# Optimization experiments

Measured on AMD Instinct MI355X. Metric: run time of the kernel, lower is better.

Reference implementation:

```python
import jax, jax.numpy as jnp
import numpy as np

N = 100000   # nodes
E = 800000   # edges
P = 100000   # pos/neg pairs
H = 4        # heads
IN = 128     # input feature dim
HID = 32     # per-head out dim (H*HID = 128)


def gat_layer(h, src, dst, W, al, ar, b):
    """DGL-style GATConv: gather -> leaky_relu attention -> segment softmax -> scatter."""
    n = h.shape[0]
    nh, nf = al.shape
    feat = (h @ W).reshape(n, nh, nf)                       # [N,H,F]
    el = jnp.einsum('nhf,hf->nh', feat, al)                 # [N,H]
    er = jnp.einsum('nhf,hf->nh', feat, ar)                 # [N,H]
    e = jax.nn.leaky_relu(el[src] + er[dst], negative_slope=0.2)  # [E,H]
    emax = jax.ops.segment_max(e, dst, num_segments=n)      # [N,H]
    emax = jnp.where(jnp.isfinite(emax), emax, 0.0)         # zero-in-degree guard
    w = jnp.exp(e - emax[dst])                              # [E,H]
    denom = jax.ops.segment_sum(w, dst, num_segments=n)     # [N,H]
    alpha = w / jnp.maximum(denom[dst], 1e-9)               # [E,H]
    out = jax.ops.segment_sum(feat[src] * alpha[:, :, None], dst, num_segments=n)  # [N,H,F]
    return out.reshape(n, nh * nf) + b


def setup_inputs() -> dict:
    key = jax.random.key(0)
    ks = jax.random.split(key, 32)
    s = 0.1
    d = {
        'x': jax.random.normal(ks[0], (N, IN), jnp.float32),
        'src': jax.random.randint(ks[1], (E,), 0, N),
        'dst': jax.random.randint(ks[2], (E,), 0, N),
        'pos_src': jax.random.randint(ks[3], (P,), 0, N),
        'pos_dst': jax.random.randint(ks[4], (P,), 0, N),
        'neg_src': jax.random.randint(ks[5], (P,), 0, N),
        'neg_dst': jax.random.randint(ks[6], (P,), 0, N),
    }
    HF = H * HID
    # 3 GATConv layers, all 128 -> 4x32
    for l in range(3):
        ind = IN if l == 0 else HF
        d[f'W{l}'] = s * jax.random.normal(ks[7 + 4 * l], (ind, HF), jnp.float32)
        d[f'al{l}'] = s * jax.random.normal(ks[8 + 4 * l], (H, HID), jnp.float32)
        d[f'ar{l}'] = s * jax.random.normal(ks[9 + 4 * l], (H, HID), jnp.float32)
        d[f'b{l}'] = jnp.zeros((HF,), jnp.float32)
    # projection 128 -> 32
    d['Wp'] = s * jax.random.normal(ks[20], (HF, HID), jnp.float32)
    d['bp'] = jnp.zeros((HID,), jnp.float32)
    # predictor MLP 32 -> 32 -> 32 -> 1
    d['Wq1'] = s * jax.random.normal(ks[21], (HID, HID), jnp.float32)
    d['bq1'] = jnp.zeros((HID,), jnp.float32)
    d['Wq2'] = s * jax.random.normal(ks[22], (HID, HID), jnp.float32)
    d['bq2'] = jnp.zeros((HID,), jnp.float32)
    d['Wq3'] = s * jax.random.normal(ks[23], (HID, 1), jnp.float32)
    d['bq3'] = jnp.zeros((1,), jnp.float32)
    return d


def reference(x, src, dst, pos_src, pos_dst, neg_src, neg_dst,
              W0, al0, ar0, b0, W1, al1, ar1, b1, W2, al2, ar2, b2,
              Wp, bp, Wq1, bq1, Wq2, bq2, Wq3, bq3):
    h = x
    for W, al, ar, b in ((W0, al0, ar0, b0), (W1, al1, ar1, b1), (W2, al2, ar2, b2)):
        h = jax.nn.elu(gat_layer(h, src, dst, W, al, ar, b))
    h = h @ Wp + bp                                          # [N,HID]

    def predictor(z):
        z = jax.nn.relu(z @ Wq1 + bq1)
        z = jax.nn.relu(z @ Wq2 + bq2)
        return z @ Wq3 + bq3

    h_pos = predictor(h[pos_src] * h[pos_dst])               # [P,1]
    h_neg = predictor(h[neg_src] * h[neg_dst])               # [P,1]
    return (h_pos, h_neg)
```

## Files before the change

kernel.cpp:

```cpp
#include <hip/hip_runtime.h>
#include <math.h>

__global__ __launch_bounds__(256) void hist_k(const int* __restrict__ dst, int* __restrict__ deg, int e) {
    int i = blockIdx.x * 256 + threadIdx.x;
    if (i < e) atomicAdd(&deg[dst[i]], 1);
}

__global__ __launch_bounds__(256) void scan1_k(const int* __restrict__ deg, int* __restrict__ rowptr,
                                               int* __restrict__ bsum, int n) {
    __shared__ int sh[256];
    int tid = threadIdx.x;
    int sid = blockIdx.x * 256 + tid;
    int v = (sid < n) ? deg[sid] : 0;
    sh[tid] = v; __syncthreads();
    for (int off = 1; off < 256; off <<= 1) {
        int t = (tid >= off) ? sh[tid - off] : 0;
        __syncthreads();
        sh[tid] += t;
        __syncthreads();
    }
    if (sid < n) rowptr[sid + 1] = sh[tid];
    if (tid == 255) bsum[blockIdx.x] = sh[255];
}

__global__ __launch_bounds__(512) void scan2_k(int* __restrict__ bsum, int nb) {
    __shared__ int sh[512];
    int tid = threadIdx.x;
    sh[tid] = (tid < nb) ? bsum[tid] : 0;
    __syncthreads();
    for (int off = 1; off < 512; off <<= 1) {
        int t = (tid >= off) ? sh[tid - off] : 0;
        __syncthreads();
        sh[tid] += t;
        __syncthreads();
    }
    if (tid < nb) bsum[tid] = sh[tid];
}

__global__ __launch_bounds__(256) void scan3_k(int* __restrict__ rowptr, const int* __restrict__ bsum, int n) {
    int sid = blockIdx.x * 256 + threadIdx.x;
    if (sid == 0) rowptr[0] = 0;
    if (sid < n && blockIdx.x > 0) rowptr[sid + 1] += bsum[blockIdx.x - 1];
}

__global__ __launch_bounds__(256) void fill_k(const int* __restrict__ src, const int* __restrict__ dst,
                                              const int* __restrict__ rowptr, int* __restrict__ cursor,
                                              int* __restrict__ csrc, int* __restrict__ cdst, int e) {
    int i = blockIdx.x * 256 + threadIdx.x;
    if (i < e) {
        int d = dst[i];
        int pos = rowptr[d] + atomicAdd(&cursor[d], 1);
        csrc[pos] = src[i];
        cdst[pos] = d;
    }
}

__global__ __launch_bounds__(256) void gemm_feat_k(const float* __restrict__ A, const float* __restrict__ W,
                                                   const float* __restrict__ al, const float* __restrict__ ar,
                                                   float* __restrict__ C, float* __restrict__ el,
                                                   float* __restrict__ er, int M) {
    __shared__ float As[32][132];
    __shared__ float Bs[32][128];
    int tid = threadIdx.x;
    int m0 = blockIdx.x * 128;
    int tr = tid >> 4;
    int tc = tid & 15;
    float4 alA = *(const float4*)(al + tc * 4);
    float4 alB = *(const float4*)(al + 64 + tc * 4);
    float4 arA = *(const float4*)(ar + tc * 4);
    float4 arB = *(const float4*)(ar + 64 + tc * 4);
    float acc[8][8];
    #pragma unroll
    for (int i = 0; i < 8; i++)
        #pragma unroll
        for (int j = 0; j < 8; j++) acc[i][j] = 0.f;

    int arow = tid >> 3, acg = tid & 7;
    int bkr = tid >> 5, bcg = tid & 31;

    for (int kb = 0; kb < 128; kb += 32) {
        #pragma unroll
        for (int rp = 0; rp < 4; ++rp) {
            int m = m0 + arow + rp * 32;
            int mm = min(m, M - 1);
            float4 a4 = *(const float4*)(A + (size_t)mm * 128 + kb + acg * 4);
            As[acg * 4 + 0][arow + rp * 32] = a4.x;
            As[acg * 4 + 1][arow + rp * 32] = a4.y;
            As[acg * 4 + 2][arow + rp * 32] = a4.z;
            As[acg * 4 + 3][arow + rp * 32] = a4.w;
        }
        #pragma unroll
        for (int rp = 0; rp < 4; ++rp) {
            int k = kb + bkr + rp * 8;
            *(float4*)&Bs[bkr + rp * 8][bcg * 4] = *(const float4*)(W + (size_t)k * 128 + bcg * 4);
        }
        __syncthreads();
        #pragma unroll
        for (int k = 0; k < 32; ++k) {
            float a[8], b[8];
            *(float4*)(a)     = *(float4*)&As[k][tr * 4];
            *(float4*)(a + 4) = *(float4*)&As[k][64 + tr * 4];
            *(float4*)(b)     = *(float4*)&Bs[k][tc * 4];
            *(float4*)(b + 4) = *(float4*)&Bs[k][64 + tc * 4];
            #pragma unroll
            for (int i = 0; i < 8; i++)
                #pragma unroll
                for (int j = 0; j < 8; j++) acc[i][j] += a[i] * b[j];
        }
        __syncthreads();
    }
    #pragma unroll
    for (int i = 0; i < 8; i++) {
        int m = m0 + ((i < 4) ? (tr * 4 + i) : (64 + tr * 4 + (i - 4)));
        if (m < M) {
            *(float4*)(C + (size_t)m * 128 + tc * 4)      = make_float4(acc[i][0], acc[i][1], acc[i][2], acc[i][3]);
            *(float4*)(C + (size_t)m * 128 + 64 + tc * 4) = make_float4(acc[i][4], acc[i][5], acc[i][6], acc[i][7]);
        }
    }
    #pragma unroll
    for (int i = 0; i < 8; i++) {
        float plA = acc[i][0] * alA.x + acc[i][1] * alA.y + acc[i][2] * alA.z + acc[i][3] * alA.w;
        float plB = acc[i][4] * alB.x + acc[i][5] * alB.y + acc[i][6] * alB.z + acc[i][7] * alB.w;
        float prA = acc[i][0] * arA.x + acc[i][1] * arA.y + acc[i][2] * arA.z + acc[i][3] * arA.w;
        float prB = acc[i][4] * arB.x + acc[i][5] * arB.y + acc[i][6] * arB.z + acc[i][7] * arB.w;
        #pragma unroll
        for (int off = 1; off < 8; off <<= 1) {
            plA += __shfl_xor(plA, off);
            plB += __shfl_xor(plB, off);
            prA += __shfl_xor(prA, off);
            prB += __shfl_xor(prB, off);
        }
        if ((tc & 7) == 0) {
            int m = m0 + ((i < 4) ? (tr * 4 + i) : (64 + tr * 4 + (i - 4)));
            if (m < M) {
                int hA = tc >> 3;
                el[m * 4 + hA]     = plA;
                el[m * 4 + hA + 2] = plB;
                er[m * 4 + hA]     = prA;
                er[m * 4 + hA + 2] = prB;
            }
        }
    }
}

__global__ __launch_bounds__(256) void edgew_k(const int* __restrict__ csrc, const int* __restrict__ cdst,
                                               const float* __restrict__ el, const float* __restrict__ er,
                                               float* __restrict__ wbuf, int e) {
    int p = blockIdx.x * 256 + threadIdx.x;
    if (p >= e) return;
    int s = csrc[p], d = cdst[p];
    float4 l4 = *(const float4*)(el + (size_t)s * 4);
    float4 r4 = *(const float4*)(er + (size_t)d * 4);
    float e0 = l4.x + r4.x, e1 = l4.y + r4.y, e2 = l4.z + r4.z, e3 = l4.w + r4.w;
    e0 = (e0 > 0.f) ? e0 : 0.2f * e0;
    e1 = (e1 > 0.f) ? e1 : 0.2f * e1;
    e2 = (e2 > 0.f) ? e2 : 0.2f * e2;
    e3 = (e3 > 0.f) ? e3 : 0.2f * e3;
    *(float4*)(wbuf + (size_t)p * 4) = make_float4(__expf(e0), __expf(e1), __expf(e2), __expf(e3));
}

__global__ __launch_bounds__(256) void aggregate_k(const float* __restrict__ feat, const float* __restrict__ wbuf,
                                                   const int* __restrict__ rowptr, const int* __restrict__ csrc,
                                                   const float* __restrict__ bias, float* __restrict__ out, int n) {
    int wid = threadIdx.x >> 6;
    int lane = threadIdx.x & 63;
    int node = blockIdx.x * 4 + wid;
    if (node >= n) return;
    int h = lane >> 4;
    int p0 = rowptr[node], p1 = rowptr[node + 1];
    float2 b2 = *(const float2*)(bias + lane * 2);
    float lsum = 0.f, a0 = 0.f, a1 = 0.f;
    int p = p0;
    for (; p + 4 <= p1; p += 4) {
        int s0 = csrc[p], s1 = csrc[p + 1], s2 = csrc[p + 2], s3 = csrc[p + 3];
        float w0 = wbuf[(size_t)p * 4 + h];
        float w1 = wbuf[(size_t)(p + 1) * 4 + h];
        float w2 = wbuf[(size_t)(p + 2) * 4 + h];
        float w3 = wbuf[(size_t)(p + 3) * 4 + h];
        float2 f0 = *(const float2*)(feat + (size_t)s0 * 128 + lane * 2);
        float2 f1 = *(const float2*)(feat + (size_t)s1 * 128 + lane * 2);
        float2 f2 = *(const float2*)(feat + (size_t)s2 * 128 + lane * 2);
        float2 f3 = *(const float2*)(feat + (size_t)s3 * 128 + lane * 2);
        lsum += (w0 + w1) + (w2 + w3);
        a0 += w0 * f0.x + w1 * f1.x + w2 * f2.x + w3 * f3.x;
        a1 += w0 * f0.y + w1 * f1.y + w2 * f2.y + w3 * f3.y;
    }
    for (; p < p1; ++p) {
        int s = csrc[p];
        float w = wbuf[(size_t)p * 4 + h];
        float2 f = *(const float2*)(feat + (size_t)s * 128 + lane * 2);
        lsum += w;
        a0 += w * f.x;
        a1 += w * f.y;
    }
    float inv = 1.f / fmaxf(lsum, 1e-9f);
    float v0 = a0 * inv + b2.x;
    float v1 = a1 * inv + b2.y;
    v0 = (v0 > 0.f) ? v0 : expm1f(v0);
    v1 = (v1 > 0.f) ? v1 : expm1f(v1);
    *(float2*)(out + (size_t)node * 128 + lane * 2) = make_float2(v0, v1);
}

__global__ __launch_bounds__(256) void proj_k(const float* __restrict__ h, const float* __restrict__ Wp,
                                              const float* __restrict__ bp, float* __restrict__ hp, int n) {
    __shared__ float Ws[128 * 32];
    __shared__ float Hs[32][132];
    int tid = threadIdx.x;
    for (int i = tid; i < 4096; i += 256) Ws[i] = Wp[i];
    int n0 = blockIdx.x * 32;
    for (int i = tid; i < 1024; i += 256) {
        int r = i >> 5, c4 = i & 31;
        int node = n0 + r;
        float4 v = (node < n) ? *(const float4*)(h + (size_t)node * 128 + c4 * 4)
                              : make_float4(0.f, 0.f, 0.f, 0.f);
        *(float4*)&Hs[r][c4 * 4] = v;
    }
    __syncthreads();
    int r = tid >> 3;
    int node = n0 + r;
    int j0 = (tid & 7) * 4;
    if (node < n) {
        float a0 = bp[j0], a1 = bp[j0 + 1], a2 = bp[j0 + 2], a3 = bp[j0 + 3];
        #pragma unroll
        for (int k = 0; k < 128; k++) {
            float av = Hs[r][k];
            float4 w = *(const float4*)&Ws[k * 32 + j0];
            a0 += av * w.x; a1 += av * w.y; a2 += av * w.z; a3 += av * w.w;
        }
        *(float4*)(hp + (size_t)node * 32 + j0) = make_float4(a0, a1, a2, a3);
    }
}

__global__ __launch_bounds__(256) void predictor_k(const float* __restrict__ hp,
                                                   const int* __restrict__ ps, const int* __restrict__ pd,
                                                   const int* __restrict__ ns, const int* __restrict__ nd,
                                                   const float* __restrict__ Wq1, const float* __restrict__ bq1,
                                                   const float* __restrict__ Wq2, const float* __restrict__ bq2,
                                                   const float* __restrict__ Wq3, const float* __restrict__ bq3,
                                                   float* __restrict__ out, int P) {
    __shared__ float w1[1024], w2[1024], w3[32], b1[32], b2[32];
    int tid = threadIdx.x;
    for (int i = tid; i < 1024; i += 256) { w1[i] = Wq1[i]; w2[i] = Wq2[i]; }
    if (tid < 32) { w3[tid] = Wq3[tid]; b1[tid] = bq1[tid]; b2[tid] = bq2[tid]; }
    __syncthreads();
    int gid = blockIdx.x * 256 + tid;
    if (gid >= 2 * P) return;
    int i = (gid < P) ? gid : gid - P;
    int a = (gid < P) ? ps[i] : ns[i];
    int b = (gid < P) ? pd[i] : nd[i];
    float z[32];
    const float4* ha = (const float4*)(hp + (size_t)a * 32);
    const float4* hb = (const float4*)(hp + (size_t)b * 32);
    #pragma unroll
    for (int q = 0; q < 8; q++) {
        float4 x = ha[q], y = hb[q];
        z[q * 4 + 0] = x.x * y.x; z[q * 4 + 1] = x.y * y.y;
        z[q * 4 + 2] = x.z * y.z; z[q * 4 + 3] = x.w * y.w;
    }
    float z1[32];
    #pragma unroll
    for (int j = 0; j < 32; j++) {
        float s = b1[j];
        #pragma unroll
        for (int k = 0; k < 32; k++) s += z[k] * w1[k * 32 + j];
        z1[j] = fmaxf(s, 0.f);
    }
    #pragma unroll
    for (int j = 0; j < 32; j++) {
        float s = b2[j];
        #pragma unroll
        for (int k = 0; k < 32; k++) s += z1[k] * w2[k * 32 + j];
        z[j] = fmaxf(s, 0.f);
    }
    float s3 = bq3[0];
    #pragma unroll
    for (int j = 0; j < 32; j++) s3 += z[j] * w3[j];
    out[gid] = s3;
}

extern "C" void kernel_launch(void* const* d_in, const int* in_sizes, int n_in,
                              void* d_out, int out_size, void* d_ws, size_t ws_size,
                              hipStream_t stream) {
    const float* x   = (const float*)d_in[0];
    const int* src   = (const int*)d_in[1];
    const int* dst   = (const int*)d_in[2];
    const int* psrc  = (const int*)d_in[3];
    const int* pdst  = (const int*)d_in[4];
    const int* nsrc  = (const int*)d_in[5];
    const int* ndst  = (const int*)d_in[6];
    const float* W[3]  = { (const float*)d_in[7],  (const float*)d_in[11], (const float*)d_in[15] };
    const float* al[3] = { (const float*)d_in[8],  (const float*)d_in[12], (const float*)d_in[16] };
    const float* ar[3] = { (const float*)d_in[9],  (const float*)d_in[13], (const float*)d_in[17] };
    const float* bb[3] = { (const float*)d_in[10], (const float*)d_in[14], (const float*)d_in[18] };
    const float* Wp  = (const float*)d_in[19];
    const float* bp  = (const float*)d_in[20];
    const float* Wq1 = (const float*)d_in[21];
    const float* bq1 = (const float*)d_in[22];
    const float* Wq2 = (const float*)d_in[23];
    const float* bq2 = (const float*)d_in[24];
    const float* Wq3 = (const float*)d_in[25];
    const float* bq3 = (const float*)d_in[26];
    float* out = (float*)d_out;

    const int N = in_sizes[0] / 128;
    const int E = in_sizes[1];
    const int P = in_sizes[3];

    size_t off = 0;
    auto alloc = [&](size_t bytes) {
        void* p = (char*)d_ws + off;
        off += (bytes + 255) & ~(size_t)255;
        return p;
    };
    float* bufF  = (float*)alloc((size_t)N * 128 * 4);
    float* bufH  = (float*)alloc((size_t)N * 128 * 4);
    float* elA   = (float*)alloc((size_t)N * 4 * 4);
    float* erA   = (float*)alloc((size_t)N * 4 * 4);
    float* hp    = (float*)alloc((size_t)N * 32 * 4);
    int* rowptr  = (int*)alloc((size_t)(N + 1) * 4);
    int* csrc    = (int*)alloc((size_t)E * 4);
    int* cdst    = (int*)alloc((size_t)E * 4);
    float* wbuf  = (float*)alloc((size_t)E * 4 * 4);
    int* deg     = (int*)alloc((size_t)N * 4);
    int* cursor  = (int*)alloc((size_t)N * 4);
    int* bsum    = (int*)alloc(1024 * 4);
    (void)ws_size;

    const int NB_E = (E + 255) / 256;
    const int NB_N = (N + 255) / 256;

    hipMemsetAsync(deg, 0, (size_t)N * 4, stream);
    hipMemsetAsync(cursor, 0, (size_t)N * 4, stream);

    hist_k<<<NB_E, 256, 0, stream>>>(dst, deg, E);
    scan1_k<<<NB_N, 256, 0, stream>>>(deg, rowptr, bsum, N);
    scan2_k<<<1, 512, 0, stream>>>(bsum, NB_N);
    scan3_k<<<NB_N, 256, 0, stream>>>(rowptr, bsum, N);
    fill_k<<<NB_E, 256, 0, stream>>>(src, dst, rowptr, cursor, csrc, cdst, E);

    const int GEMM_B = (N + 127) / 128;
    const float* hin = x;
    for (int l = 0; l < 3; l++) {
        gemm_feat_k<<<GEMM_B, 256, 0, stream>>>(hin, W[l], al[l], ar[l], bufF, elA, erA, N);
        edgew_k<<<NB_E, 256, 0, stream>>>(csrc, cdst, elA, erA, wbuf, E);
        aggregate_k<<<(N + 3) / 4, 256, 0, stream>>>(bufF, wbuf, rowptr, csrc, bb[l], bufH, N);
        hin = bufH;
    }
    proj_k<<<(N + 31) / 32, 256, 0, stream>>>(bufH, Wp, bp, hp, N);
    predictor_k<<<(2 * P + 255) / 256, 256, 0, stream>>>(hp, psrc, pdst, nsrc, ndst,
                                                         Wq1, bq1, Wq2, bq2, Wq3, bq3, out, P);
}
```

Measured before the change: 558.1 us.

## Halve GEMM tile rows and add register prefetch of next k-tile

The feature GEMM now uses 64-row tiles with 128-thread blocks instead of 128-row tiles with 256 threads. Global loads for the next k-slice of A and W go into registers while the current slice is computed from shared memory. The aim is to hide global load latency and raise occupancy with more, smaller blocks. The cost is more register pressure and twice as many reloads of W across blocks.

```diff
diff --git a/kernel.cpp b/kernel.cpp
--- a/kernel.cpp
+++ b/kernel.cpp
@@ -55,14 +55,14 @@
     }
 }
 
-__global__ __launch_bounds__(256) void gemm_feat_k(const float* __restrict__ A, const float* __restrict__ W,
-                                                   const float* __restrict__ al, const float* __restrict__ ar,
-                                                   float* __restrict__ C, float* __restrict__ el,
-                                                   float* __restrict__ er, int M) {
-    __shared__ float As[32][132];
+__global__ __launch_bounds__(128, 3) void gemm_feat_k(const float* __restrict__ A, const float* __restrict__ W,
+                                                      const float* __restrict__ al, const float* __restrict__ ar,
+                                                      float* __restrict__ C, float* __restrict__ el,
+                                                      float* __restrict__ er, int M) {
+    __shared__ float As[32][68];
     __shared__ float Bs[32][128];
     int tid = threadIdx.x;
-    int m0 = blockIdx.x * 128;
+    int m0 = blockIdx.x * 64;
     int tr = tid >> 4;
     int tc = tid & 15;
     float4 alA = *(const float4*)(al + tc * 4);
@@ -75,31 +75,43 @@
         #pragma unroll
         for (int j = 0; j < 8; j++) acc[i][j] = 0.f;
 
-    int arow = tid >> 3, acg = tid & 7;
+    int arow = tid >> 1, acg = tid & 1;
     int bkr = tid >> 5, bcg = tid & 31;
 
+    int mm = min(m0 + arow, M - 1);
+    const float* Arow = A + (size_t)mm * 128;
+
+    float4 pa[4], pb[8];
+    #pragma unroll
+    for (int j = 0; j < 4; j++) pa[j] = *(const float4*)(Arow + (acg * 4 + j) * 4);
+    #pragma unroll
+    for (int rp = 0; rp < 8; rp++) pb[rp] = *(const float4*)(W + (size_t)(rp * 4 + bkr) * 128 + bcg * 4);
+
     for (int kb = 0; kb < 128; kb += 32) {
         #pragma unroll
-        for (int rp = 0; rp < 4; ++rp) {
-            int m = m0 + arow + rp * 32;
-            int mm = min(m, M - 1);
-            float4 a4 = *(const float4*)(A + (size_t)mm * 128 + kb + acg * 4);
-            As[acg * 4 + 0][arow + rp * 32] = a4.x;
-            As[acg * 4 + 1][arow + rp * 32] = a4.y;
-            As[acg * 4 + 2][arow + rp * 32] = a4.z;
-            As[acg * 4 + 3][arow + rp * 32] = a4.w;
-        }
-        #pragma unroll
-        for (int rp = 0; rp < 4; ++rp) {
-            int k = kb + bkr + rp * 8;
-            *(float4*)&Bs[bkr + rp * 8][bcg * 4] = *(const float4*)(W + (size_t)k * 128 + bcg * 4);
-        }
-        __syncthreads();
+        for (int j = 0; j < 4; j++) {
+            int kr = acg * 16 + j * 4;
+            As[kr + 0][arow] = pa[j].x;
+            As[kr + 1][arow] = pa[j].y;
+            As[kr + 2][arow] = pa[j].z;
+            As[kr + 3][arow] = pa[j].w;
+        }
+        #pragma unroll
+        for (int rp = 0; rp < 8; rp++)
+            *(float4*)&Bs[rp * 4 + bkr][bcg * 4] = pb[rp];
+        __syncthreads();
+        if (kb < 96) {
+            int kn = kb + 32;
+            #pragma unroll
+            for (int j = 0; j < 4; j++) pa[j] = *(const float4*)(Arow + kn + (acg * 4 + j) * 4);
+            #pragma unroll
+            for (int rp = 0; rp < 8; rp++) pb[rp] = *(const float4*)(W + (size_t)(kn + rp * 4 + bkr) * 128 + bcg * 4);
+        }
         #pragma unroll
         for (int k = 0; k < 32; ++k) {
             float a[8], b[8];
             *(float4*)(a)     = *(float4*)&As[k][tr * 4];
-            *(float4*)(a + 4) = *(float4*)&As[k][64 + tr * 4];
+            *(float4*)(a + 4) = *(float4*)&As[k][32 + tr * 4];
             *(float4*)(b)     = *(float4*)&Bs[k][tc * 4];
             *(float4*)(b + 4) = *(float4*)&Bs[k][64 + tc * 4];
             #pragma unroll
@@ -111,7 +123,7 @@
     }
     #pragma unroll
     for (int i = 0; i < 8; i++) {
-        int m = m0 + ((i < 4) ? (tr * 4 + i) : (64 + tr * 4 + (i - 4)));
+        int m = m0 + ((i < 4) ? (tr * 4 + i) : (32 + tr * 4 + (i - 4)));
         if (m < M) {
             *(float4*)(C + (size_t)m * 128 + tc * 4)      = make_float4(acc[i][0], acc[i][1], acc[i][2], acc[i][3]);
             *(float4*)(C + (size_t)m * 128 + 64 + tc * 4) = make_float4(acc[i][4], acc[i][5], acc[i][6], acc[i][7]);
@@ -131,7 +143,7 @@
             prB += __shfl_xor(prB, off);
         }
         if ((tc & 7) == 0) {
-            int m = m0 + ((i < 4) ? (tr * 4 + i) : (64 + tr * 4 + (i - 4)));
+            int m = m0 + ((i < 4) ? (tr * 4 + i) : (32 + tr * 4 + (i - 4)));
             if (m < M) {
                 int hA = tc >> 3;
                 el[m * 4 + hA]     = plA;
@@ -338,10 +350,10 @@
     scan3_k<<<NB_N, 256, 0, stream>>>(rowptr, bsum, N);
     fill_k<<<NB_E, 256, 0, stream>>>(src, dst, rowptr, cursor, csrc, cdst, E);
 
-    const int GEMM_B = (N + 127) / 128;
+    const int GEMM_B = (N + 63) / 64;
     const float* hin = x;
     for (int l = 0; l < 3; l++) {
-        gemm_feat_k<<<GEMM_B, 256, 0, stream>>>(hin, W[l], al[l], ar[l], bufF, elA, erA, N);
+        gemm_feat_k<<<GEMM_B, 128, 0, stream>>>(hin, W[l], al[l], ar[l], bufF, elA, erA, N);
         edgew_k<<<NB_E, 256, 0, stream>>>(csrc, cdst, elA, erA, wbuf, E);
         aggregate_k<<<(N + 3) / 4, 256, 0, stream>>>(bufF, wbuf, rowptr, csrc, bb[l], bufH, N);
         hin = bufH;
```

Result: slower. 1.064 ms (+90.7%).

## Replace FP32 SIMT feature GEMM with split-bf16 MFMA GEMM

Applied to the files above, without the earlier changes.

Replaces the shared-memory FP32 FMA GEMM for the per-layer feature transform with a matrix-core kernel using bf16 MFMA instructions. Accuracy is preserved by splitting both A and W into high and low bf16 parts and issuing three MFMAs per tile (hi*hi, lo*hi, hi*lo). A small kernel pre-converts and transposes W into the two bf16 halves each layer. The attention projections el/er are fused in the epilogue using cross-lane shuffles. This trades extra MFMA work and per-element conversion for moving the GEMM off scalar FMAs, and it drops LDS staging in favour of direct global loads.

```diff
diff --git a/kernel.cpp b/kernel.cpp
--- a/kernel.cpp
+++ b/kernel.cpp
@@ -1,5 +1,14 @@
 #include <hip/hip_runtime.h>
 #include <math.h>
+
+typedef __attribute__((ext_vector_type(8))) short bf16x8;
+typedef __attribute__((ext_vector_type(4))) float f32x4;
+
+__device__ __forceinline__ unsigned short f2bf_rtne(float v) {
+    unsigned u = __float_as_uint(v);
+    u += 0x7FFFu + ((u >> 16) & 1u);
+    return (unsigned short)(u >> 16);
+}
 
 __global__ __launch_bounds__(256) void hist_k(const int* __restrict__ dst, int* __restrict__ deg, int e) {
     int i = blockIdx.x * 256 + threadIdx.x;
@@ -55,89 +64,109 @@
     }
 }
 
-__global__ __launch_bounds__(256) void gemm_feat_k(const float* __restrict__ A, const float* __restrict__ W,
-                                                   const float* __restrict__ al, const float* __restrict__ ar,
-                                                   float* __restrict__ C, float* __restrict__ el,
-                                                   float* __restrict__ er, int M) {
-    __shared__ float As[32][132];
-    __shared__ float Bs[32][128];
-    int tid = threadIdx.x;
-    int m0 = blockIdx.x * 128;
-    int tr = tid >> 4;
-    int tc = tid & 15;
-    float4 alA = *(const float4*)(al + tc * 4);
-    float4 alB = *(const float4*)(al + 64 + tc * 4);
-    float4 arA = *(const float4*)(ar + tc * 4);
-    float4 arB = *(const float4*)(ar + 64 + tc * 4);
-    float acc[8][8];
-    #pragma unroll
-    for (int i = 0; i < 8; i++)
-        #pragma unroll
-        for (int j = 0; j < 8; j++) acc[i][j] = 0.f;
-
-    int arow = tid >> 3, acg = tid & 7;
-    int bkr = tid >> 5, bcg = tid & 31;
-
-    for (int kb = 0; kb < 128; kb += 32) {
-        #pragma unroll
-        for (int rp = 0; rp < 4; ++rp) {
-            int m = m0 + arow + rp * 32;
-            int mm = min(m, M - 1);
-            float4 a4 = *(const float4*)(A + (size_t)mm * 128 + kb + acg * 4);
-            As[acg * 4 + 0][arow + rp * 32] = a4.x;
-            As[acg * 4 + 1][arow + rp * 32] = a4.y;
-            As[acg * 4 + 2][arow + rp * 32] = a4.z;
-            As[acg * 4 + 3][arow + rp * 32] = a4.w;
-        }
-        #pragma unroll
-        for (int rp = 0; rp < 4; ++rp) {
-            int k = kb + bkr + rp * 8;
-            *(float4*)&Bs[bkr + rp * 8][bcg * 4] = *(const float4*)(W + (size_t)k * 128 + bcg * 4);
-        }
-        __syncthreads();
-        #pragma unroll
-        for (int k = 0; k < 32; ++k) {
-            float a[8], b[8];
-            *(float4*)(a)     = *(float4*)&As[k][tr * 4];
-            *(float4*)(a + 4) = *(float4*)&As[k][64 + tr * 4];
-            *(float4*)(b)     = *(float4*)&Bs[k][tc * 4];
-            *(float4*)(b + 4) = *(float4*)&Bs[k][64 + tc * 4];
+__global__ __launch_bounds__(256) void wconv_k(const float* __restrict__ W,
+                                               unsigned short* __restrict__ Wth,
+                                               unsigned short* __restrict__ Wtl) {
+    int idx = blockIdx.x * 256 + threadIdx.x;
+    int k = idx >> 7, n = idx & 127;
+    float v = W[idx];
+    unsigned short h = f2bf_rtne(v);
+    float hf = __uint_as_float((unsigned)h << 16);
+    Wth[n * 128 + k] = h;
+    Wtl[n * 128 + k] = f2bf_rtne(v - hf);
+}
+
+__global__ __launch_bounds__(256) void gemm_mfma_k(const float* __restrict__ A,
+        const unsigned short* __restrict__ Wth, const unsigned short* __restrict__ Wtl,
+        const float* __restrict__ alp, const float* __restrict__ arp,
+        float* __restrict__ C, float* __restrict__ el, float* __restrict__ er, int M) {
+    int tid = threadIdx.x;
+    int wv = tid >> 6, lane = tid & 63;
+    int l15 = lane & 15, lhi = lane >> 4;
+    int mb = blockIdx.x * 128 + wv * 32;
+
+    f32x4 acc[2][8];
+    #pragma unroll
+    for (int f = 0; f < 2; f++)
+        #pragma unroll
+        for (int n = 0; n < 8; n++) acc[f][n] = (f32x4){0.f, 0.f, 0.f, 0.f};
+
+    float alv[8], arv[8];
+    #pragma unroll
+    for (int n = 0; n < 8; n++) { alv[n] = alp[n * 16 + l15]; arv[n] = arp[n * 16 + l15]; }
+
+    int r0 = mb + l15, r1 = mb + 16 + l15;
+    const float* a0p = A + (size_t)min(r0, M - 1) * 128 + lhi * 8;
+    const float* a1p = A + (size_t)min(r1, M - 1) * 128 + lhi * 8;
+
+    #pragma unroll
+    for (int ks = 0; ks < 4; ks++) {
+        int kb = ks * 32 + lhi * 8;
+        float av[8];
+        bf16x8 a0h, a0l, a1h, a1l;
+        *(float4*)(av)     = *(const float4*)(a0p + ks * 32);
+        *(float4*)(av + 4) = *(const float4*)(a0p + ks * 32 + 4);
+        #pragma unroll
+        for (int j = 0; j < 8; j++) {
+            unsigned short h = f2bf_rtne(av[j]);
+            a0h[j] = (short)h;
+            a0l[j] = (short)f2bf_rtne(av[j] - __uint_as_float((unsigned)h << 16));
+        }
+        *(float4*)(av)     = *(const float4*)(a1p + ks * 32);
+        *(float4*)(av + 4) = *(const float4*)(a1p + ks * 32 + 4);
+        #pragma unroll
+        for (int j = 0; j < 8; j++) {
+            unsigned short h = f2bf_rtne(av[j]);
+            a1h[j] = (short)h;
+            a1l[j] = (short)f2bf_rtne(av[j] - __uint_as_float((unsigned)h << 16));
+        }
+        #pragma unroll
+        for (int n = 0; n < 8; n++) {
+            bf16x8 bhv = *(const bf16x8*)(Wth + (size_t)(n * 16 + l15) * 128 + kb);
+            bf16x8 blv = *(const bf16x8*)(Wtl + (size_t)(n * 16 + l15) * 128 + kb);
+            acc[0][n] = __builtin_amdgcn_mfma_f32_16x16x32_bf16(a0h, bhv, acc[0][n], 0, 0, 0);
+            acc[1][n] = __builtin_amdgcn_mfma_f32_16x16x32_bf16(a1h, bhv, acc[1][n], 0, 0, 0);
+            acc[0][n] = __builtin_amdgcn_mfma_f32_16x16x32_bf16(a0l, bhv, acc[0][n], 0, 0, 0);
+            acc[1][n] = __builtin_amdgcn_mfma_f32_16x16x32_bf16(a1l, bhv, acc[1][n], 0, 0, 0);
+            acc[0][n] = __builtin_amdgcn_mfma_f32_16x16x32_bf16(a0h, blv, acc[0][n], 0, 0, 0);
+            acc[1][n] = __builtin_amdgcn_mfma_f32_16x16x32_bf16(a1h, blv, acc[1][n], 0, 0, 0);
+        }
+    }
+
+    #pragma unroll
+    for (int f = 0; f < 2; f++) {
+        #pragma unroll
+        for (int i = 0; i < 4; i++) {
+            int r = mb + f * 16 + lhi * 4 + i;
+            bool ok = (r < M);
+            if (ok) {
+                #pragma unroll
+                for (int n = 0; n < 8; n++)
+                    C[(size_t)r * 128 + n * 16 + l15] = acc[f][n][i];
+            }
+            float ph[4], qh[4];
             #pragma unroll
-            for (int i = 0; i < 8; i++)
+            for (int h = 0; h < 4; h++) {
+                ph[h] = acc[f][2 * h][i] * alv[2 * h] + acc[f][2 * h + 1][i] * alv[2 * h + 1];
+                qh[h] = acc[f][2 * h][i] * arv[2 * h] + acc[f][2 * h + 1][i] * arv[2 * h + 1];
+            }
+            #pragma unroll
+            for (int off = 1; off < 16; off <<= 1) {
                 #pragma unroll
-                for (int j = 0; j < 8; j++) acc[i][j] += a[i] * b[j];
-        }
-        __syncthreads();
-    }
-    #pragma unroll
-    for (int i = 0; i < 8; i++) {
-        int m = m0 + ((i < 4) ? (tr * 4 + i) : (64 + tr * 4 + (i - 4)));
-        if (m < M) {
-            *(float4*)(C + (size_t)m * 128 + tc * 4)      = make_float4(acc[i][0], acc[i][1], acc[i][2], acc[i][3]);
-            *(float4*)(C + (size_t)m * 128 + 64 + tc * 4) = make_float4(acc[i][4], acc[i][5], acc[i][6], acc[i][7]);
-        }
-    }
-    #pragma unroll
-    for (int i = 0; i < 8; i++) {
-        float plA = acc[i][0] * alA.x + acc[i][1] * alA.y + acc[i][2] * alA.z + acc[i][3] * alA.w;
-        float plB = acc[i][4] * alB.x + acc[i][5] * alB.y + acc[i][6] * alB.z + acc[i][7] * alB.w;
-        float prA = acc[i][0] * arA.x + acc[i][1] * arA.y + acc[i][2] * arA.z + acc[i][3] * arA.w;
-        float prB = acc[i][4] * arB.x + acc[i][5] * arB.y + acc[i][6] * arB.z + acc[i][7] * arB.w;
-        #pragma unroll
-        for (int off = 1; off < 8; off <<= 1) {
-            plA += __shfl_xor(plA, off);
-            plB += __shfl_xor(plB, off);
-            prA += __shfl_xor(prA, off);
-            prB += __shfl_xor(prB, off);
-        }
-        if ((tc & 7) == 0) {
-            int m = m0 + ((i < 4) ? (tr * 4 + i) : (64 + tr * 4 + (i - 4)));
-            if (m < M) {
-                int hA = tc >> 3;
-                el[m * 4 + hA]     = plA;
-                el[m * 4 + hA + 2] = plB;
-                er[m * 4 + hA]     = prA;
-                er[m * 4 + hA + 2] = prB;
+                for (int h = 0; h < 4; h++) {
+                    ph[h] += __shfl_xor(ph[h], off);
+                    qh[h] += __shfl_xor(qh[h], off);
+                }
+            }
+            if (ok && l15 < 8) {
+                if (l15 < 4) {
+                    float v = (l15 == 0) ? ph[0] : (l15 == 1) ? ph[1] : (l15 == 2) ? ph[2] : ph[3];
+                    el[(size_t)r * 4 + l15] = v;
+                } else {
+                    int h = l15 - 4;
+                    float v = (h == 0) ? qh[0] : (h == 1) ? qh[1] : (h == 2) ? qh[2] : qh[3];
+                    er[(size_t)r * 4 + h] = v;
+                }
             }
         }
     }
@@ -324,6 +353,8 @@
     int* deg     = (int*)alloc((size_t)N * 4);
     int* cursor  = (int*)alloc((size_t)N * 4);
     int* bsum    = (int*)alloc(1024 * 4);
+    unsigned short* Wth = (unsigned short*)alloc(16384 * 2);
+    unsigned short* Wtl = (unsigned short*)alloc(16384 * 2);
     (void)ws_size;
 
     const int NB_E = (E + 255) / 256;
@@ -341,7 +372,8 @@
     const int GEMM_B = (N + 127) / 128;
     const float* hin = x;
     for (int l = 0; l < 3; l++) {
-        gemm_feat_k<<<GEMM_B, 256, 0, stream>>>(hin, W[l], al[l], ar[l], bufF, elA, erA, N);
+        wconv_k<<<64, 256, 0, stream>>>(W[l], Wth, Wtl);
+        gemm_mfma_k<<<GEMM_B, 256, 0, stream>>>(hin, Wth, Wtl, al[l], ar[l], bufF, elA, erA, N);
         edgew_k<<<NB_E, 256, 0, stream>>>(csrc, cdst, elA, erA, wbuf, E);
         aggregate_k<<<(N + 3) / 4, 256, 0, stream>>>(bufF, wbuf, rowptr, csrc, bb[l], bufH, N);
         hin = bufH;
```

Measured after the change: 557.5 us. Within noise of the previous version (-0.1%).
